# Performance work log

Measured on AMD Instinct MI355X. Metric: run time of the kernel, lower is better.

## Reference

```python
import jax, jax.numpy as jnp
import numpy as np

H, N, F = 10, 200000, 128
HID, C = 256, 100
NEG_SLOPE = 0.2

def _leaky(x):
    return jnp.where(x >= 0, x, NEG_SLOPE * x)

def _prelu(x, a):
    return jnp.where(x >= 0, x, a * x)

def setup_inputs() -> dict:
    key = jax.random.key(0)
    ks = jax.random.split(key, 12)
    inp = {
        "features": jax.random.normal(ks[0], (H, N, F), dtype=jnp.float32),
        "label_emb": jax.random.normal(ks[1], (N, C), dtype=jnp.float32),
        # lr_att: Linear(2F, 1) -> weight as [2F] vector + scalar bias
        "W_att": jax.random.normal(ks[2], (2 * F,), dtype=jnp.float32) * 0.05,
        "b_att": jnp.zeros((), dtype=jnp.float32),
        # lr_output = FeedForwardNetII(F, HID, C, n_layers=2): Dense(F,HID), PReLU, Dense(HID,C)
        "Wo1": jax.random.normal(ks[3], (F, HID), dtype=jnp.float32) * 0.05,
        "bo1": jnp.zeros((HID,), dtype=jnp.float32),
        "ao": jnp.asarray(0.25, dtype=jnp.float32),
        "Wo2": jax.random.normal(ks[4], (HID, C), dtype=jnp.float32) * 0.05,
        "bo2": jnp.zeros((C,), dtype=jnp.float32),
        # label_fc = FeedForwardNet(C, HID, C, n_layers=2): Linear(C,HID), PReLU, Linear(HID,C)
        "Wl1": jax.random.normal(ks[5], (C, HID), dtype=jnp.float32) * 0.05,
        "bl1": jnp.zeros((HID,), dtype=jnp.float32),
        "al": jnp.asarray(0.25, dtype=jnp.float32),
        "Wl2": jax.random.normal(ks[6], (HID, C), dtype=jnp.float32) * 0.05,
        "bl2": jnp.zeros((C,), dtype=jnp.float32),
    }
    return inp

def reference(features, label_emb, W_att, b_att, Wo1, bo1, ao, Wo2, bo2,
              Wl1, bl1, al, Wl2, bl2):
    # features: [H, N, F]; dropouts are identity (p=0, eval mode)
    nF = features.shape[-1]
    W1, W2 = W_att[:nF], W_att[nF:]  # cat([history, x_i]) @ W_att == history@W1 + x_i@W2
    x0 = features[0]
    scores = [_leaky(x0 @ (W1 + W2) + b_att)]  # hop 0: cat([x0, x0])
    for i in range(1, features.shape[0]):
        hist_att = jax.nn.softmax(jnp.stack(scores, axis=1), axis=1)  # [N, i]
        history = jnp.einsum('ni,inf->nf', hist_att, features[:i])    # [N, F]
        scores.append(_leaky(history @ W1 + features[i] @ W2 + b_att))
    att = jax.nn.softmax(jnp.stack(scores, axis=1), axis=1)           # [N, H]
    right = jnp.einsum('ni,inf->nf', att, features)                   # [N, F]
    # lr_output: Dense -> PReLU -> Dense
    out = _prelu(right @ Wo1 + bo1, ao) @ Wo2 + bo2                   # [N, C]
    # label branch: label_fc(label_emb)
    out = out + (_prelu(label_emb @ Wl1 + bl1, al) @ Wl2 + bl2)
    return out
```

## Files before the change

### kernel.cpp

```cpp
#include <hip/hip_runtime.h>
#include <cstddef>

#define NHOP 10
#define NN 200000
#define FF 128
#define HIDD 256
#define CCC 100
#define NEG_SLOPE_C 0.2f

typedef __attribute__((ext_vector_type(8))) short bf16x8;
typedef __attribute__((ext_vector_type(4))) short bf16x4;
typedef __attribute__((ext_vector_type(4))) float f32x4;

__device__ __forceinline__ unsigned short f2bf(float x){
  unsigned u = __float_as_uint(x);
  u = u + 0x7FFFu + ((u >> 16) & 1u);
  return (unsigned short)(u >> 16);
}

__device__ __forceinline__ f32x4 mfma16(bf16x8 a, bf16x8 b, f32x4 c){
  return __builtin_amdgcn_mfma_f32_16x16x32_bf16(a, b, c, 0, 0, 0);
}

__device__ __forceinline__ float leakyf(float x){ return x >= 0.f ? x : NEG_SLOPE_C*x; }

__global__ __launch_bounds__(256) void prep_weights(
    const float* __restrict__ Wo1, const float* __restrict__ Wl1,
    const float* __restrict__ Wo2, const float* __restrict__ Wl2,
    unsigned short* __restrict__ Wo1T, unsigned short* __restrict__ Wl1T,
    unsigned short* __restrict__ Wo2T, unsigned short* __restrict__ Wl2T)
{
  const int id = blockIdx.x*256 + threadIdx.x;
  {
    const int c = id >> 7, k = id & 127;
    Wo1T[id] = f2bf(Wo1[(size_t)k*HIDD + c]);
    Wl1T[id] = (k < CCC) ? f2bf(Wl1[(size_t)k*HIDD + c]) : 0;
  }
  if (id < 112*256){
    const int c = id >> 8, k = id & 255;
    Wo2T[id] = (c < CCC) ? f2bf(Wo2[(size_t)k*CCC + c]) : 0;
    Wl2T[id] = (c < CCC) ? f2bf(Wl2[(size_t)k*CCC + c]) : 0;
  }
}

__global__ __launch_bounds__(256) void attn_right_kernel(
    const float* __restrict__ feat,
    const float* __restrict__ Watt,
    const float* __restrict__ batt,
    unsigned short* __restrict__ rightb)
{
  const int lane = threadIdx.x & 63;
  const int n = blockIdx.x * 4 + (threadIdx.x >> 6);
  if (n >= NN) return;

  const float2 w1 = *reinterpret_cast<const float2*>(Watt + 2*lane);
  const float2 w2 = *reinterpret_cast<const float2*>(Watt + FF + 2*lane);
  const float b = batt[0];

  float2 f[NHOP];
  float p1[NHOP], p2[NHOP];
  const float* fp = feat + (size_t)n*FF + 2*lane;
  #pragma unroll
  for (int i=0;i<NHOP;i++){
    f[i] = *reinterpret_cast<const float2*>(fp + (size_t)i*((size_t)NN*FF));
    p1[i] = f[i].x*w1.x + f[i].y*w1.y;
    p2[i] = f[i].x*w2.x + f[i].y*w2.y;
  }
  #pragma unroll
  for (int m=32;m>0;m>>=1){
    #pragma unroll
    for (int i=0;i<NHOP;i++){
      p1[i] += __shfl_xor(p1[i], m, 64);
      p2[i] += __shfl_xor(p2[i], m, 64);
    }
  }
  float sc[NHOP];
  sc[0] = leakyf(p1[0] + p2[0] + b);
  #pragma unroll
  for (int i=1;i<NHOP;i++){
    float mx = sc[0];
    #pragma unroll
    for (int j=1;j<i;j++) mx = fmaxf(mx, sc[j]);
    float Z = 0.f, hs = 0.f;
    #pragma unroll
    for (int j=0;j<i;j++){
      const float e = __expf(sc[j]-mx);
      Z += e;
      hs = fmaf(e, p1[j], hs);
    }
    sc[i] = leakyf(hs/Z + p2[i] + b);
  }
  float mx = sc[0];
  #pragma unroll
  for (int j=1;j<NHOP;j++) mx = fmaxf(mx, sc[j]);
  float Z = 0.f;
  float e[NHOP];
  #pragma unroll
  for (int j=0;j<NHOP;j++){ e[j] = __expf(sc[j]-mx); Z += e[j]; }
  const float inv = 1.f/Z;
  float rx = 0.f, ry = 0.f;
  #pragma unroll
  for (int j=0;j<NHOP;j++){
    const float a = e[j]*inv;
    rx = fmaf(a, f[j].x, rx);
    ry = fmaf(a, f[j].y, ry);
  }
  ushort2 st; st.x = f2bf(rx); st.y = f2bf(ry);
  *reinterpret_cast<ushort2*>(rightb + (size_t)n*FF + 2*lane) = st;
}

__device__ __forceinline__ void mlp_branch(
    const unsigned short* sA, unsigned short* sH,
    const unsigned short* __restrict__ W1T, const float* __restrict__ b1, const float alpha,
    const unsigned short* __restrict__ W2T,
    f32x4 (&o)[2][4], const int w, const int lr, const int lq)
{
  bf16x8 B[4][4];
  float b1c[4];
  #pragma unroll
  for (int ctl=0; ctl<4; ++ctl){
    const int c = (4*w+ctl)*16 + lr;
    b1c[ctl] = b1[c];
    #pragma unroll
    for (int kk=0; kk<4; ++kk)
      B[ctl][kk] = *reinterpret_cast<const bf16x8*>(W1T + (size_t)c*128 + kk*32 + lq*8);
  }
  #pragma unroll
  for (int nt=0; nt<4; ++nt){
    f32x4 h[4];
    #pragma unroll
    for (int ctl=0; ctl<4; ++ctl) h[ctl] = (f32x4){0.f,0.f,0.f,0.f};
    const int row = nt*16 + lr;
    #pragma unroll
    for (int kk=0; kk<4; ++kk){
      const bf16x8 a = *reinterpret_cast<const bf16x8*>(
          (const char*)sA + row*256 + ((kk*64 + lq*16) ^ ((row&7)<<4)));
      #pragma unroll
      for (int ctl=0; ctl<4; ++ctl)
        h[ctl] = mfma16(a, B[ctl][kk], h[ctl]);
    }
    #pragma unroll
    for (int ctl=0; ctl<4; ++ctl){
      const int c = (4*w+ctl)*16 + lr;
      #pragma unroll
      for (int j=0; j<4; ++j){
        float v = h[ctl][j] + b1c[ctl];
        v = v >= 0.f ? v : alpha*v;
        const int n = nt*16 + lq*4 + j;
        *reinterpret_cast<unsigned short*>(
            (char*)sH + n*512 + ((2*c) ^ ((n&7)<<4))) = f2bf(v);
      }
    }
  }
  __syncthreads();
  #pragma unroll
  for (int i2=0; i2<2; ++i2){
    const int ct2 = 2*w + i2;
    if (ct2 < 7){
      bf16x8 b2[8];
      #pragma unroll
      for (int kk=0; kk<8; ++kk)
        b2[kk] = *reinterpret_cast<const bf16x8*>(W2T + (size_t)(ct2*16+lr)*256 + kk*32 + lq*8);
      #pragma unroll
      for (int nt=0; nt<4; ++nt){
        const int row = nt*16 + lr;
        #pragma unroll
        for (int kk=0; kk<8; ++kk){
          const bf16x8 a2 = *reinterpret_cast<const bf16x8*>(
              (const char*)sH + row*512 + ((kk*64 + lq*16) ^ ((row&7)<<4)));
          o[i2][nt] = mfma16(a2, b2[kk], o[i2][nt]);
        }
      }
    }
  }
}

__global__ __launch_bounds__(256) void mlp_mfma_kernel(
    const unsigned short* __restrict__ rightb, const float* __restrict__ label,
    const unsigned short* __restrict__ Wo1T, const float* __restrict__ bo1, const float* __restrict__ aop,
    const unsigned short* __restrict__ Wo2T, const float* __restrict__ bo2,
    const unsigned short* __restrict__ Wl1T, const float* __restrict__ bl1, const float* __restrict__ alp,
    const unsigned short* __restrict__ Wl2T, const float* __restrict__ bl2,
    float* __restrict__ out)
{
  __shared__ __align__(16) unsigned short sA[64*128];
  __shared__ __align__(16) unsigned short sH[64*256];
  const int t = threadIdx.x;
  const int w = t >> 6, lane = t & 63, lr = lane & 15, lq = lane >> 4;
  const size_t nb = (size_t)blockIdx.x * 64;

  f32x4 o[2][4];
  #pragma unroll
  for (int i2=0; i2<2; ++i2){
    const int ct2 = 2*w + i2;
    const int c2 = ct2*16 + lr;
    const float init = (ct2 < 7 && c2 < CCC) ? (bo2[c2] + bl2[c2]) : 0.f;
    #pragma unroll
    for (int nt=0; nt<4; ++nt) o[i2][nt] = (f32x4){init, init, init, init};
  }

  {
    const unsigned short* src = rightb + nb*FF;
    #pragma unroll
    for (int i=0;i<4;i++){
      const int chunk = t + 256*i;
      const int row = chunk >> 4, cs = chunk & 15;
      const bf16x8 v = *reinterpret_cast<const bf16x8*>(src + row*FF + cs*8);
      *reinterpret_cast<bf16x8*>((char*)sA + row*256 + ((cs*16) ^ ((row&7)<<4))) = v;
    }
  }
  __syncthreads();
  mlp_branch(sA, sH, Wo1T, bo1, aop[0], Wo2T, o, w, lr, lq);

  {
    #pragma unroll
    for (int i=0;i<7;i++){
      const int idx = t + 256*i;
      if (idx < 1600){
        const int row = idx/25, c0 = (idx%25)*4;
        const float4 v = *reinterpret_cast<const float4*>(label + (nb+row)*CCC + c0);
        bf16x4 p;
        p[0] = (short)f2bf(v.x); p[1] = (short)f2bf(v.y);
        p[2] = (short)f2bf(v.z); p[3] = (short)f2bf(v.w);
        *reinterpret_cast<bf16x4*>((char*)sA + row*256 + ((2*c0) ^ ((row&7)<<4))) = p;
      }
    }
    for (int idx = t; idx < 448; idx += 256){
      const int row = idx/7, ch = idx%7;
      *reinterpret_cast<bf16x4*>((char*)sA + row*256 + ((200 + 8*ch) ^ ((row&7)<<4))) = (bf16x4){0,0,0,0};
    }
  }
  __syncthreads();
  mlp_branch(sA, sH, Wl1T, bl1, alp[0], Wl2T, o, w, lr, lq);

  #pragma unroll
  for (int i2=0; i2<2; ++i2){
    const int ct2 = 2*w + i2;
    const int c2 = ct2*16 + lr;
    if (ct2 < 7 && c2 < CCC){
      #pragma unroll
      for (int nt=0; nt<4; ++nt){
        #pragma unroll
        for (int j=0; j<4; ++j){
          const int n = nt*16 + lq*4 + j;
          out[(nb + n)*CCC + c2] = o[i2][nt][j];
        }
      }
    }
  }
}

extern "C" void kernel_launch(void* const* d_in, const int* in_sizes, int n_in,
                              void* d_out, int out_size, void* d_ws, size_t ws_size,
                              hipStream_t stream) {
  const float* feat  = (const float*)d_in[0];
  const float* label = (const float*)d_in[1];
  const float* Watt  = (const float*)d_in[2];
  const float* batt  = (const float*)d_in[3];
  const float* Wo1   = (const float*)d_in[4];
  const float* bo1   = (const float*)d_in[5];
  const float* aop   = (const float*)d_in[6];
  const float* Wo2   = (const float*)d_in[7];
  const float* bo2   = (const float*)d_in[8];
  const float* Wl1   = (const float*)d_in[9];
  const float* bl1   = (const float*)d_in[10];
  const float* alp   = (const float*)d_in[11];
  const float* Wl2   = (const float*)d_in[12];
  const float* bl2   = (const float*)d_in[13];
  float* out = (float*)d_out;

  unsigned short* rightb = (unsigned short*)d_ws;
  unsigned short* Wo1T = rightb + (size_t)NN*FF;
  unsigned short* Wl1T = Wo1T + 256*128;
  unsigned short* Wo2T = Wl1T + 256*128;
  unsigned short* Wl2T = Wo2T + 112*256;

  prep_weights<<<128, 256, 0, stream>>>(Wo1, Wl1, Wo2, Wl2, Wo1T, Wl1T, Wo2T, Wl2T);
  attn_right_kernel<<<NN/4, 256, 0, stream>>>(feat, Watt, batt, rightb);
  mlp_mfma_kernel<<<NN/64, 256, 0, stream>>>(rightb, label,
                                             Wo1T, bo1, aop, Wo2T, bo2,
                                             Wl1T, bl1, alp, Wl2T, bl2, out);
}
```

Baseline: 416.9 us.

## Pack hop features as bf16 in attention kernel and drop MLP staging buffer

```diff
diff --git a/kernel.cpp b/kernel.cpp
--- a/kernel.cpp
+++ b/kernel.cpp
@@ -17,6 +17,9 @@
   u = u + 0x7FFFu + ((u >> 16) & 1u);
   return (unsigned short)(u >> 16);
 }
+__device__ __forceinline__ float bf2f(short s){
+  return __uint_as_float(((unsigned)(unsigned short)s) << 16);
+}
 
 __device__ __forceinline__ f32x4 mfma16(bf16x8 a, bf16x8 b, f32x4 c){
   return __builtin_amdgcn_mfma_f32_16x16x32_bf16(a, b, c, 0, 0, 0);
@@ -50,24 +53,35 @@
     unsigned short* __restrict__ rightb)
 {
   const int lane = threadIdx.x & 63;
-  const int n = blockIdx.x * 4 + (threadIdx.x >> 6);
-  if (n >= NN) return;
-
-  const float2 w1 = *reinterpret_cast<const float2*>(Watt + 2*lane);
-  const float2 w2 = *reinterpret_cast<const float2*>(Watt + FF + 2*lane);
+  const int w = threadIdx.x >> 6;
+  const int nl = lane >> 4, fl = lane & 15;
+  const int n = blockIdx.x*16 + w*4 + nl;
+
+  const float4 w1a = *reinterpret_cast<const float4*>(Watt + fl*4);
+  const float4 w1b = *reinterpret_cast<const float4*>(Watt + 64 + fl*4);
+  const float4 w2a = *reinterpret_cast<const float4*>(Watt + FF + fl*4);
+  const float4 w2b = *reinterpret_cast<const float4*>(Watt + FF + 64 + fl*4);
   const float b = batt[0];
 
-  float2 f[NHOP];
   float p1[NHOP], p2[NHOP];
-  const float* fp = feat + (size_t)n*FF + 2*lane;
+  bf16x8 fbf[NHOP];
+  const float* fp = feat + (size_t)n*FF;
   #pragma unroll
   for (int i=0;i<NHOP;i++){
-    f[i] = *reinterpret_cast<const float2*>(fp + (size_t)i*((size_t)NN*FF));
-    p1[i] = f[i].x*w1.x + f[i].y*w1.y;
-    p2[i] = f[i].x*w2.x + f[i].y*w2.y;
-  }
-  #pragma unroll
-  for (int m=32;m>0;m>>=1){
+    const float* hp = fp + (size_t)i*((size_t)NN*FF);
+    const float4 va = *reinterpret_cast<const float4*>(hp + fl*4);
+    const float4 vb = *reinterpret_cast<const float4*>(hp + 64 + fl*4);
+    p1[i] = va.x*w1a.x + va.y*w1a.y + va.z*w1a.z + va.w*w1a.w
+          + vb.x*w1b.x + vb.y*w1b.y + vb.z*w1b.z + vb.w*w1b.w;
+    p2[i] = va.x*w2a.x + va.y*w2a.y + va.z*w2a.z + va.w*w2a.w
+          + vb.x*w2b.x + vb.y*w2b.y + vb.z*w2b.z + vb.w*w2b.w;
+    fbf[i][0]=(short)f2bf(va.x); fbf[i][1]=(short)f2bf(va.y);
+    fbf[i][2]=(short)f2bf(va.z); fbf[i][3]=(short)f2bf(va.w);
+    fbf[i][4]=(short)f2bf(vb.x); fbf[i][5]=(short)f2bf(vb.y);
+    fbf[i][6]=(short)f2bf(vb.z); fbf[i][7]=(short)f2bf(vb.w);
+  }
+  #pragma unroll
+  for (int m=8;m>0;m>>=1){
     #pragma unroll
     for (int i=0;i<NHOP;i++){
       p1[i] += __shfl_xor(p1[i], m, 64);
@@ -98,61 +112,40 @@
   #pragma unroll
   for (int j=0;j<NHOP;j++){ e[j] = __expf(sc[j]-mx); Z += e[j]; }
   const float inv = 1.f/Z;
-  float rx = 0.f, ry = 0.f;
+  float racc[8];
+  #pragma unroll
+  for (int u=0;u<8;u++) racc[u] = 0.f;
   #pragma unroll
   for (int j=0;j<NHOP;j++){
     const float a = e[j]*inv;
-    rx = fmaf(a, f[j].x, rx);
-    ry = fmaf(a, f[j].y, ry);
-  }
-  ushort2 st; st.x = f2bf(rx); st.y = f2bf(ry);
-  *reinterpret_cast<ushort2*>(rightb + (size_t)n*FF + 2*lane) = st;
-}
-
-__device__ __forceinline__ void mlp_branch(
-    const unsigned short* sA, unsigned short* sH,
-    const unsigned short* __restrict__ W1T, const float* __restrict__ b1, const float alpha,
-    const unsigned short* __restrict__ W2T,
-    f32x4 (&o)[2][4], const int w, const int lr, const int lq)
-{
-  bf16x8 B[4][4];
-  float b1c[4];
-  #pragma unroll
-  for (int ctl=0; ctl<4; ++ctl){
-    const int c = (4*w+ctl)*16 + lr;
-    b1c[ctl] = b1[c];
-    #pragma unroll
-    for (int kk=0; kk<4; ++kk)
-      B[ctl][kk] = *reinterpret_cast<const bf16x8*>(W1T + (size_t)c*128 + kk*32 + lq*8);
-  }
-  #pragma unroll
-  for (int nt=0; nt<4; ++nt){
-    f32x4 h[4];
-    #pragma unroll
-    for (int ctl=0; ctl<4; ++ctl) h[ctl] = (f32x4){0.f,0.f,0.f,0.f};
-    const int row = nt*16 + lr;
-    #pragma unroll
-    for (int kk=0; kk<4; ++kk){
-      const bf16x8 a = *reinterpret_cast<const bf16x8*>(
-          (const char*)sA + row*256 + ((kk*64 + lq*16) ^ ((row&7)<<4)));
-      #pragma unroll
-      for (int ctl=0; ctl<4; ++ctl)
-        h[ctl] = mfma16(a, B[ctl][kk], h[ctl]);
-    }
-    #pragma unroll
-    for (int ctl=0; ctl<4; ++ctl){
-      const int c = (4*w+ctl)*16 + lr;
-      #pragma unroll
-      for (int j=0; j<4; ++j){
-        float v = h[ctl][j] + b1c[ctl];
-        v = v >= 0.f ? v : alpha*v;
-        const int n = nt*16 + lq*4 + j;
-        *reinterpret_cast<unsigned short*>(
-            (char*)sH + n*512 + ((2*c) ^ ((n&7)<<4))) = f2bf(v);
-      }
-    }
-  }
-  __syncthreads();
+    #pragma unroll
+    for (int u=0;u<8;u++) racc[u] = fmaf(a, bf2f(fbf[j][u]), racc[u]);
+  }
+  bf16x4 sa, sb;
+  sa[0]=(short)f2bf(racc[0]); sa[1]=(short)f2bf(racc[1]);
+  sa[2]=(short)f2bf(racc[2]); sa[3]=(short)f2bf(racc[3]);
+  sb[0]=(short)f2bf(racc[4]); sb[1]=(short)f2bf(racc[5]);
+  sb[2]=(short)f2bf(racc[6]); sb[3]=(short)f2bf(racc[7]);
+  *reinterpret_cast<bf16x4*>(rightb + (size_t)n*FF + fl*4) = sa;
+  *reinterpret_cast<bf16x4*>(rightb + (size_t)n*FF + 64 + fl*4) = sb;
+}
+
+__device__ __forceinline__ void scatter_h(unsigned short* sH, f32x4 h, float bias,
+                                          float alpha, int c, int nt, int lq)
+{
+  #pragma unroll
+  for (int j=0;j<4;++j){
+    float v = h[j] + bias;
+    v = v >= 0.f ? v : alpha*v;
+    const int n = nt*16 + lq*4 + j;
+    *reinterpret_cast<unsigned short*>((char*)sH + n*512 + ((2*c) ^ ((n&7)<<4))) = f2bf(v);
+  }
+}
+
+__device__ __forceinline__ void gemm2_accum(const unsigned short* sH,
+    const unsigned short* __restrict__ W2T, f32x4 (&o)[2][4],
+    const int w, const int lr, const int lq)
+{
   #pragma unroll
   for (int i2=0; i2<2; ++i2){
     const int ct2 = 2*w + i2;
@@ -175,6 +168,23 @@
   }
 }
 
+__device__ __forceinline__ bf16x8 label_frag(const float* __restrict__ label,
+                                             size_t gnode, int kk, int lq)
+{
+  bf16x8 r = (bf16x8){0,0,0,0,0,0,0,0};
+  const float* base = label + gnode*CCC;
+  if (kk < 3){
+    const float4 va = *reinterpret_cast<const float4*>(base + kk*32 + lq*8);
+    const float4 vb = *reinterpret_cast<const float4*>(base + kk*32 + lq*8 + 4);
+    r[0]=(short)f2bf(va.x); r[1]=(short)f2bf(va.y); r[2]=(short)f2bf(va.z); r[3]=(short)f2bf(va.w);
+    r[4]=(short)f2bf(vb.x); r[5]=(short)f2bf(vb.y); r[6]=(short)f2bf(vb.z); r[7]=(short)f2bf(vb.w);
+  } else if (lq == 0){
+    const float4 va = *reinterpret_cast<const float4*>(base + 96);
+    r[0]=(short)f2bf(va.x); r[1]=(short)f2bf(va.y); r[2]=(short)f2bf(va.z); r[3]=(short)f2bf(va.w);
+  }
+  return r;
+}
+
 __global__ __launch_bounds__(256) void mlp_mfma_kernel(
     const unsigned short* __restrict__ rightb, const float* __restrict__ label,
     const unsigned short* __restrict__ Wo1T, const float* __restrict__ bo1, const float* __restrict__ aop,
@@ -183,11 +193,11 @@
     const unsigned short* __restrict__ Wl2T, const float* __restrict__ bl2,
     float* __restrict__ out)
 {
-  __shared__ __align__(16) unsigned short sA[64*128];
   __shared__ __align__(16) unsigned short sH[64*256];
   const int t = threadIdx.x;
   const int w = t >> 6, lane = t & 63, lr = lane & 15, lq = lane >> 4;
   const size_t nb = (size_t)blockIdx.x * 64;
+  const float ao = aop[0], al = alp[0];
 
   f32x4 o[2][4];
   #pragma unroll
@@ -199,39 +209,65 @@
     for (int nt=0; nt<4; ++nt) o[i2][nt] = (f32x4){init, init, init, init};
   }
 
-  {
-    const unsigned short* src = rightb + nb*FF;
-    #pragma unroll
-    for (int i=0;i<4;i++){
-      const int chunk = t + 256*i;
-      const int row = chunk >> 4, cs = chunk & 15;
-      const bf16x8 v = *reinterpret_cast<const bf16x8*>(src + row*FF + cs*8);
-      *reinterpret_cast<bf16x8*>((char*)sA + row*256 + ((cs*16) ^ ((row&7)<<4))) = v;
+  #pragma unroll
+  for (int cc=0; cc<2; ++cc){
+    bf16x8 B[2][4];
+    float b1c[2];
+    #pragma unroll
+    for (int ct=0; ct<2; ++ct){
+      const int c = (w*4 + cc*2 + ct)*16 + lr;
+      b1c[ct] = bo1[c];
+      #pragma unroll
+      for (int kk=0; kk<4; ++kk)
+        B[ct][kk] = *reinterpret_cast<const bf16x8*>(Wo1T + (size_t)c*128 + kk*32 + lq*8);
+    }
+    #pragma unroll
+    for (int nt=0; nt<4; ++nt){
+      const int row = nt*16 + lr;
+      f32x4 h0 = (f32x4){0.f,0.f,0.f,0.f}, h1 = h0;
+      #pragma unroll
+      for (int kk=0; kk<4; ++kk){
+        const bf16x8 a = *reinterpret_cast<const bf16x8*>(
+            rightb + (nb + row)*FF + kk*32 + lq*8);
+        h0 = mfma16(a, B[0][kk], h0);
+        h1 = mfma16(a, B[1][kk], h1);
+      }
+      scatter_h(sH, h0, b1c[0], ao, (w*4 + cc*2 + 0)*16 + lr, nt, lq);
+      scatter_h(sH, h1, b1c[1], ao, (w*4 + cc*2 + 1)*16 + lr, nt, lq);
     }
   }
   __syncthreads();
-  mlp_branch(sA, sH, Wo1T, bo1, aop[0], Wo2T, o, w, lr, lq);
-
-  {
-    #pragma unroll
-    for (int i=0;i<7;i++){
-      const int idx = t + 256*i;
-      if (idx < 1600){
-        const int row = idx/25, c0 = (idx%25)*4;
-        const float4 v = *reinterpret_cast<const float4*>(label + (nb+row)*CCC + c0);
-        bf16x4 p;
-        p[0] = (short)f2bf(v.x); p[1] = (short)f2bf(v.y);
-        p[2] = (short)f2bf(v.z); p[3] = (short)f2bf(v.w);
-        *reinterpret_cast<bf16x4*>((char*)sA + row*256 + ((2*c0) ^ ((row&7)<<4))) = p;
+  gemm2_accum(sH, Wo2T, o, w, lr, lq);
+  __syncthreads();
+
+  #pragma unroll
+  for (int cc=0; cc<2; ++cc){
+    bf16x8 B[2][4];
+    float b1c[2];
+    #pragma unroll
+    for (int ct=0; ct<2; ++ct){
+      const int c = (w*4 + cc*2 + ct)*16 + lr;
+      b1c[ct] = bl1[c];
+      #pragma unroll
+      for (int kk=0; kk<4; ++kk)
+        B[ct][kk] = *reinterpret_cast<const bf16x8*>(Wl1T + (size_t)c*128 + kk*32 + lq*8);
+    }
+    #pragma unroll
+    for (int nt=0; nt<4; ++nt){
+      const int row = nt*16 + lr;
+      f32x4 h0 = (f32x4){0.f,0.f,0.f,0.f}, h1 = h0;
+      #pragma unroll
+      for (int kk=0; kk<4; ++kk){
+        const bf16x8 a = label_frag(label, nb + row, kk, lq);
+        h0 = mfma16(a, B[0][kk], h0);
+        h1 = mfma16(a, B[1][kk], h1);
       }
-    }
-    for (int idx = t; idx < 448; idx += 256){
-      const int row = idx/7, ch = idx%7;
-      *reinterpret_cast<bf16x4*>((char*)sA + row*256 + ((200 + 8*ch) ^ ((row&7)<<4))) = (bf16x4){0,0,0,0};
+      scatter_h(sH, h0, b1c[0], al, (w*4 + cc*2 + 0)*16 + lr, nt, lq);
+      scatter_h(sH, h1, b1c[1], al, (w*4 + cc*2 + 1)*16 + lr, nt, lq);
     }
   }
   __syncthreads();
-  mlp_branch(sA, sH, Wl1T, bl1, alp[0], Wl2T, o, w, lr, lq);
+  gemm2_accum(sH, Wl2T, o, w, lr, lq);
 
   #pragma unroll
   for (int i2=0; i2<2; ++i2){
@@ -276,7 +312,7 @@
   unsigned short* Wl2T = Wo2T + 112*256;
 
   prep_weights<<<128, 256, 0, stream>>>(Wo1, Wl1, Wo2, Wl2, Wo1T, Wl1T, Wo2T, Wl2T);
-  attn_right_kernel<<<NN/4, 256, 0, stream>>>(feat, Watt, batt, rightb);
+  attn_right_kernel<<<NN/16, 256, 0, stream>>>(feat, Watt, batt, rightb);
   mlp_mfma_kernel<<<NN/64, 256, 0, stream>>>(rightb, label,
                                              Wo1T, bo1, aop, Wo2T, bo2,
                                              Wl1T, bl1, alp, Wl2T, bl2, out);
```

New measurement: 400.3 us. 4.0% less time.

## Load MLP A-fragments directly from global and stage output through LDS

Applied to the files above, without the earlier changes.

```diff
diff --git a/kernel.cpp b/kernel.cpp
--- a/kernel.cpp
+++ b/kernel.cpp
@@ -1,4 +1,5 @@
 #include <hip/hip_runtime.h>
+#include <hip/hip_bf16.h>
 #include <cstddef>
 
 #define NHOP 10
@@ -12,16 +13,12 @@
 typedef __attribute__((ext_vector_type(4))) short bf16x4;
 typedef __attribute__((ext_vector_type(4))) float f32x4;
 
-__device__ __forceinline__ unsigned short f2bf(float x){
-  unsigned u = __float_as_uint(x);
-  u = u + 0x7FFFu + ((u >> 16) & 1u);
-  return (unsigned short)(u >> 16);
-}
-
+__device__ __forceinline__ short f2bfs(float x){
+  return __builtin_bit_cast(short, __float2bfloat16(x));
+}
 __device__ __forceinline__ f32x4 mfma16(bf16x8 a, bf16x8 b, f32x4 c){
   return __builtin_amdgcn_mfma_f32_16x16x32_bf16(a, b, c, 0, 0, 0);
 }
-
 __device__ __forceinline__ float leakyf(float x){ return x >= 0.f ? x : NEG_SLOPE_C*x; }
 
 __global__ __launch_bounds__(256) void prep_weights(
@@ -33,13 +30,13 @@
   const int id = blockIdx.x*256 + threadIdx.x;
   {
     const int c = id >> 7, k = id & 127;
-    Wo1T[id] = f2bf(Wo1[(size_t)k*HIDD + c]);
-    Wl1T[id] = (k < CCC) ? f2bf(Wl1[(size_t)k*HIDD + c]) : 0;
+    Wo1T[id] = (unsigned short)f2bfs(Wo1[(size_t)k*HIDD + c]);
+    Wl1T[id] = (k < CCC) ? (unsigned short)f2bfs(Wl1[(size_t)k*HIDD + c]) : 0;
   }
   if (id < 112*256){
     const int c = id >> 8, k = id & 255;
-    Wo2T[id] = (c < CCC) ? f2bf(Wo2[(size_t)k*CCC + c]) : 0;
-    Wl2T[id] = (c < CCC) ? f2bf(Wl2[(size_t)k*CCC + c]) : 0;
+    Wo2T[id] = (c < CCC) ? (unsigned short)f2bfs(Wo2[(size_t)k*CCC + c]) : 0;
+    Wl2T[id] = (c < CCC) ? (unsigned short)f2bfs(Wl2[(size_t)k*CCC + c]) : 0;
   }
 }
 
@@ -51,7 +48,6 @@
 {
   const int lane = threadIdx.x & 63;
   const int n = blockIdx.x * 4 + (threadIdx.x >> 6);
-  if (n >= NN) return;
 
   const float2 w1 = *reinterpret_cast<const float2*>(Watt + 2*lane);
   const float2 w2 = *reinterpret_cast<const float2*>(Watt + FF + 2*lane);
@@ -105,54 +101,27 @@
     rx = fmaf(a, f[j].x, rx);
     ry = fmaf(a, f[j].y, ry);
   }
-  ushort2 st; st.x = f2bf(rx); st.y = f2bf(ry);
+  ushort2 st; st.x = (unsigned short)f2bfs(rx); st.y = (unsigned short)f2bfs(ry);
   *reinterpret_cast<ushort2*>(rightb + (size_t)n*FF + 2*lane) = st;
 }
 
-__device__ __forceinline__ void mlp_branch(
-    const unsigned short* sA, unsigned short* sH,
-    const unsigned short* __restrict__ W1T, const float* __restrict__ b1, const float alpha,
-    const unsigned short* __restrict__ W2T,
-    f32x4 (&o)[2][4], const int w, const int lr, const int lq)
-{
-  bf16x8 B[4][4];
-  float b1c[4];
-  #pragma unroll
-  for (int ctl=0; ctl<4; ++ctl){
-    const int c = (4*w+ctl)*16 + lr;
-    b1c[ctl] = b1[c];
-    #pragma unroll
-    for (int kk=0; kk<4; ++kk)
-      B[ctl][kk] = *reinterpret_cast<const bf16x8*>(W1T + (size_t)c*128 + kk*32 + lq*8);
-  }
-  #pragma unroll
-  for (int nt=0; nt<4; ++nt){
-    f32x4 h[4];
-    #pragma unroll
-    for (int ctl=0; ctl<4; ++ctl) h[ctl] = (f32x4){0.f,0.f,0.f,0.f};
-    const int row = nt*16 + lr;
-    #pragma unroll
-    for (int kk=0; kk<4; ++kk){
-      const bf16x8 a = *reinterpret_cast<const bf16x8*>(
-          (const char*)sA + row*256 + ((kk*64 + lq*16) ^ ((row&7)<<4)));
-      #pragma unroll
-      for (int ctl=0; ctl<4; ++ctl)
-        h[ctl] = mfma16(a, B[ctl][kk], h[ctl]);
-    }
-    #pragma unroll
-    for (int ctl=0; ctl<4; ++ctl){
-      const int c = (4*w+ctl)*16 + lr;
-      #pragma unroll
-      for (int j=0; j<4; ++j){
-        float v = h[ctl][j] + b1c[ctl];
-        v = v >= 0.f ? v : alpha*v;
-        const int n = nt*16 + lq*4 + j;
-        *reinterpret_cast<unsigned short*>(
-            (char*)sH + n*512 + ((2*c) ^ ((n&7)<<4))) = f2bf(v);
-      }
-    }
-  }
-  __syncthreads();
+__device__ __forceinline__ void scatter_h(unsigned short* sH, f32x4 h, float bias,
+                                          float alpha, int c, int nt, int lq)
+{
+  #pragma unroll
+  for (int j=0;j<4;++j){
+    float v = h[j] + bias;
+    v = v >= 0.f ? v : alpha*v;
+    const int n = nt*16 + lq*4 + j;
+    *reinterpret_cast<unsigned short*>((char*)sH + n*512 + ((2*c) ^ ((n&7)<<4))) =
+        (unsigned short)f2bfs(v);
+  }
+}
+
+__device__ __forceinline__ void gemm2_accum(const unsigned short* sH,
+    const unsigned short* __restrict__ W2T, f32x4 (&o)[2][4],
+    const int w, const int lr, const int lq)
+{
   #pragma unroll
   for (int i2=0; i2<2; ++i2){
     const int ct2 = 2*w + i2;
@@ -175,6 +144,23 @@
   }
 }
 
+__device__ __forceinline__ bf16x8 label_frag(const float* __restrict__ label,
+                                             size_t gnode, int kk, int lq)
+{
+  bf16x8 r = (bf16x8){0,0,0,0,0,0,0,0};
+  const float* base = label + gnode*CCC;
+  if (kk < 3){
+    const float4 va = *reinterpret_cast<const float4*>(base + kk*32 + lq*8);
+    const float4 vb = *reinterpret_cast<const float4*>(base + kk*32 + lq*8 + 4);
+    r[0]=f2bfs(va.x); r[1]=f2bfs(va.y); r[2]=f2bfs(va.z); r[3]=f2bfs(va.w);
+    r[4]=f2bfs(vb.x); r[5]=f2bfs(vb.y); r[6]=f2bfs(vb.z); r[7]=f2bfs(vb.w);
+  } else if (lq == 0){
+    const float4 va = *reinterpret_cast<const float4*>(base + 96);
+    r[0]=f2bfs(va.x); r[1]=f2bfs(va.y); r[2]=f2bfs(va.z); r[3]=f2bfs(va.w);
+  }
+  return r;
+}
+
 __global__ __launch_bounds__(256) void mlp_mfma_kernel(
     const unsigned short* __restrict__ rightb, const float* __restrict__ label,
     const unsigned short* __restrict__ Wo1T, const float* __restrict__ bo1, const float* __restrict__ aop,
@@ -183,11 +169,11 @@
     const unsigned short* __restrict__ Wl2T, const float* __restrict__ bl2,
     float* __restrict__ out)
 {
-  __shared__ __align__(16) unsigned short sA[64*128];
   __shared__ __align__(16) unsigned short sH[64*256];
   const int t = threadIdx.x;
   const int w = t >> 6, lane = t & 63, lr = lane & 15, lq = lane >> 4;
   const size_t nb = (size_t)blockIdx.x * 64;
+  const float ao = aop[0], al = alp[0];
 
   f32x4 o[2][4];
   #pragma unroll
@@ -200,39 +186,76 @@
   }
 
   {
-    const unsigned short* src = rightb + nb*FF;
-    #pragma unroll
-    for (int i=0;i<4;i++){
-      const int chunk = t + 256*i;
-      const int row = chunk >> 4, cs = chunk & 15;
-      const bf16x8 v = *reinterpret_cast<const bf16x8*>(src + row*FF + cs*8);
-      *reinterpret_cast<bf16x8*>((char*)sA + row*256 + ((cs*16) ^ ((row&7)<<4))) = v;
-    }
-  }
-  __syncthreads();
-  mlp_branch(sA, sH, Wo1T, bo1, aop[0], Wo2T, o, w, lr, lq);
+    bf16x8 B1[4][4];
+    float b1c[4];
+    #pragma unroll
+    for (int q=0; q<4; ++q){
+      const int c = (w*4 + q)*16 + lr;
+      b1c[q] = bo1[c];
+      #pragma unroll
+      for (int kk=0; kk<4; ++kk)
+        B1[q][kk] = *reinterpret_cast<const bf16x8*>(Wo1T + (size_t)c*128 + kk*32 + lq*8);
+    }
+    #pragma unroll
+    for (int nt=0; nt<4; ++nt){
+      const int row = nt*16 + lr;
+      bf16x8 a[4];
+      #pragma unroll
+      for (int kk=0; kk<4; ++kk)
+        a[kk] = *reinterpret_cast<const bf16x8*>(rightb + (nb + row)*FF + kk*32 + lq*8);
+      f32x4 h[4];
+      #pragma unroll
+      for (int q=0; q<4; ++q) h[q] = (f32x4){0.f,0.f,0.f,0.f};
+      #pragma unroll
+      for (int kk=0; kk<4; ++kk)
+        #pragma unroll
+        for (int q=0; q<4; ++q)
+          h[q] = mfma16(a[kk], B1[q][kk], h[q]);
+      #pragma unroll
+      for (int q=0; q<4; ++q)
+        scatter_h(sH, h[q], b1c[q], ao, (w*4 + q)*16 + lr, nt, lq);
+    }
+  }
+  __syncthreads();
+  gemm2_accum(sH, Wo2T, o, w, lr, lq);
+  __syncthreads();
 
   {
-    #pragma unroll
-    for (int i=0;i<7;i++){
-      const int idx = t + 256*i;
-      if (idx < 1600){
-        const int row = idx/25, c0 = (idx%25)*4;
-        const float4 v = *reinterpret_cast<const float4*>(label + (nb+row)*CCC + c0);
-        bf16x4 p;
-        p[0] = (short)f2bf(v.x); p[1] = (short)f2bf(v.y);
-        p[2] = (short)f2bf(v.z); p[3] = (short)f2bf(v.w);
-        *reinterpret_cast<bf16x4*>((char*)sA + row*256 + ((2*c0) ^ ((row&7)<<4))) = p;
-      }
-    }
-    for (int idx = t; idx < 448; idx += 256){
-      const int row = idx/7, ch = idx%7;
-      *reinterpret_cast<bf16x4*>((char*)sA + row*256 + ((200 + 8*ch) ^ ((row&7)<<4))) = (bf16x4){0,0,0,0};
-    }
-  }
-  __syncthreads();
-  mlp_branch(sA, sH, Wl1T, bl1, alp[0], Wl2T, o, w, lr, lq);
-
+    bf16x8 B1[4][4];
+    float b1c[4];
+    #pragma unroll
+    for (int q=0; q<4; ++q){
+      const int c = (w*4 + q)*16 + lr;
+      b1c[q] = bl1[c];
+      #pragma unroll
+      for (int kk=0; kk<4; ++kk)
+        B1[q][kk] = *reinterpret_cast<const bf16x8*>(Wl1T + (size_t)c*128 + kk*32 + lq*8);
+    }
+    #pragma unroll
+    for (int nt=0; nt<4; ++nt){
+      const int row = nt*16 + lr;
+      bf16x8 a[4];
+      #pragma unroll
+      for (int kk=0; kk<4; ++kk)
+        a[kk] = label_frag(label, nb + row, kk, lq);
+      f32x4 h[4];
+      #pragma unroll
+      for (int q=0; q<4; ++q) h[q] = (f32x4){0.f,0.f,0.f,0.f};
+      #pragma unroll
+      for (int kk=0; kk<4; ++kk)
+        #pragma unroll
+        for (int q=0; q<4; ++q)
+          h[q] = mfma16(a[kk], B1[q][kk], h[q]);
+      #pragma unroll
+      for (int q=0; q<4; ++q)
+        scatter_h(sH, h[q], b1c[q], al, (w*4 + q)*16 + lr, nt, lq);
+    }
+  }
+  __syncthreads();
+  gemm2_accum(sH, Wl2T, o, w, lr, lq);
+  __syncthreads();
+
+  float* sF = reinterpret_cast<float*>(sH);
   #pragma unroll
   for (int i2=0; i2<2; ++i2){
     const int ct2 = 2*w + i2;
@@ -241,12 +264,16 @@
       #pragma unroll
       for (int nt=0; nt<4; ++nt){
         #pragma unroll
-        for (int j=0; j<4; ++j){
-          const int n = nt*16 + lq*4 + j;
-          out[(nb + n)*CCC + c2] = o[i2][nt][j];
-        }
+        for (int j=0; j<4; ++j)
+          sF[(nt*16 + lq*4 + j)*CCC + c2] = o[i2][nt][j];
       }
     }
+  }
+  __syncthreads();
+  #pragma unroll
+  for (int p=0; p<25; ++p){
+    const int idx = p*256 + t;
+    out[nb*CCC + idx] = sF[idx];
   }
 }
 
```

After: 473.0 us. +13.5%, slower.

## Map 16 lanes per node with float4 loads and bf16 register caching in attention

Applied to the files above, without the earlier changes.

```diff
diff --git a/kernel.cpp b/kernel.cpp
--- a/kernel.cpp
+++ b/kernel.cpp
@@ -1,4 +1,5 @@
 #include <hip/hip_runtime.h>
+#include <hip/hip_bf16.h>
 #include <cstddef>
 
 #define NHOP 10
@@ -12,16 +13,15 @@
 typedef __attribute__((ext_vector_type(4))) short bf16x4;
 typedef __attribute__((ext_vector_type(4))) float f32x4;
 
-__device__ __forceinline__ unsigned short f2bf(float x){
-  unsigned u = __float_as_uint(x);
-  u = u + 0x7FFFu + ((u >> 16) & 1u);
-  return (unsigned short)(u >> 16);
-}
-
+__device__ __forceinline__ short f2bfs(float x){
+  return __builtin_bit_cast(short, __float2bfloat16(x));
+}
+__device__ __forceinline__ float bf2f(short s){
+  return __uint_as_float(((unsigned)(unsigned short)s) << 16);
+}
 __device__ __forceinline__ f32x4 mfma16(bf16x8 a, bf16x8 b, f32x4 c){
   return __builtin_amdgcn_mfma_f32_16x16x32_bf16(a, b, c, 0, 0, 0);
 }
-
 __device__ __forceinline__ float leakyf(float x){ return x >= 0.f ? x : NEG_SLOPE_C*x; }
 
 __global__ __launch_bounds__(256) void prep_weights(
@@ -33,13 +33,13 @@
   const int id = blockIdx.x*256 + threadIdx.x;
   {
     const int c = id >> 7, k = id & 127;
-    Wo1T[id] = f2bf(Wo1[(size_t)k*HIDD + c]);
-    Wl1T[id] = (k < CCC) ? f2bf(Wl1[(size_t)k*HIDD + c]) : 0;
+    Wo1T[id] = (unsigned short)f2bfs(Wo1[(size_t)k*HIDD + c]);
+    Wl1T[id] = (k < CCC) ? (unsigned short)f2bfs(Wl1[(size_t)k*HIDD + c]) : 0;
   }
   if (id < 112*256){
     const int c = id >> 8, k = id & 255;
-    Wo2T[id] = (c < CCC) ? f2bf(Wo2[(size_t)k*CCC + c]) : 0;
-    Wl2T[id] = (c < CCC) ? f2bf(Wl2[(size_t)k*CCC + c]) : 0;
+    Wo2T[id] = (c < CCC) ? (unsigned short)f2bfs(Wo2[(size_t)k*CCC + c]) : 0;
+    Wl2T[id] = (c < CCC) ? (unsigned short)f2bfs(Wl2[(size_t)k*CCC + c]) : 0;
   }
 }
 
@@ -50,24 +50,33 @@
     unsigned short* __restrict__ rightb)
 {
   const int lane = threadIdx.x & 63;
-  const int n = blockIdx.x * 4 + (threadIdx.x >> 6);
-  if (n >= NN) return;
-
-  const float2 w1 = *reinterpret_cast<const float2*>(Watt + 2*lane);
-  const float2 w2 = *reinterpret_cast<const float2*>(Watt + FF + 2*lane);
+  const int w = threadIdx.x >> 6;
+  const int nl = lane >> 4, fl = lane & 15;
+  const int n = blockIdx.x*16 + w*4 + nl;
+
+  const float4 w1a = *reinterpret_cast<const float4*>(Watt + fl*4);
+  const float4 w1b = *reinterpret_cast<const float4*>(Watt + 64 + fl*4);
+  const float4 w2a = *reinterpret_cast<const float4*>(Watt + FF + fl*4);
+  const float4 w2b = *reinterpret_cast<const float4*>(Watt + FF + 64 + fl*4);
   const float b = batt[0];
 
-  float2 f[NHOP];
   float p1[NHOP], p2[NHOP];
-  const float* fp = feat + (size_t)n*FF + 2*lane;
+  bf16x8 fbf[NHOP];
+  const float* fp = feat + (size_t)n*FF;
   #pragma unroll
   for (int i=0;i<NHOP;i++){
-    f[i] = *reinterpret_cast<const float2*>(fp + (size_t)i*((size_t)NN*FF));
-    p1[i] = f[i].x*w1.x + f[i].y*w1.y;
-    p2[i] = f[i].x*w2.x + f[i].y*w2.y;
-  }
-  #pragma unroll
-  for (int m=32;m>0;m>>=1){
+    const float* hp = fp + (size_t)i*((size_t)NN*FF);
+    const float4 va = *reinterpret_cast<const float4*>(hp + fl*4);
+    const float4 vb = *reinterpret_cast<const float4*>(hp + 64 + fl*4);
+    p1[i] = va.x*w1a.x + va.y*w1a.y + va.z*w1a.z + va.w*w1a.w
+          + vb.x*w1b.x + vb.y*w1b.y + vb.z*w1b.z + vb.w*w1b.w;
+    p2[i] = va.x*w2a.x + va.y*w2a.y + va.z*w2a.z + va.w*w2a.w
+          + vb.x*w2b.x + vb.y*w2b.y + vb.z*w2b.z + vb.w*w2b.w;
+    fbf[i][0]=f2bfs(va.x); fbf[i][1]=f2bfs(va.y); fbf[i][2]=f2bfs(va.z); fbf[i][3]=f2bfs(va.w);
+    fbf[i][4]=f2bfs(vb.x); fbf[i][5]=f2bfs(vb.y); fbf[i][6]=f2bfs(vb.z); fbf[i][7]=f2bfs(vb.w);
+  }
+  #pragma unroll
+  for (int m=8;m>0;m>>=1){
     #pragma unroll
     for (int i=0;i<NHOP;i++){
       p1[i] += __shfl_xor(p1[i], m, 64);
@@ -98,15 +107,20 @@
   #pragma unroll
   for (int j=0;j<NHOP;j++){ e[j] = __expf(sc[j]-mx); Z += e[j]; }
   const float inv = 1.f/Z;
-  float rx = 0.f, ry = 0.f;
+  float racc[8];
+  #pragma unroll
+  for (int u=0;u<8;u++) racc[u] = 0.f;
   #pragma unroll
   for (int j=0;j<NHOP;j++){
     const float a = e[j]*inv;
-    rx = fmaf(a, f[j].x, rx);
-    ry = fmaf(a, f[j].y, ry);
-  }
-  ushort2 st; st.x = f2bf(rx); st.y = f2bf(ry);
-  *reinterpret_cast<ushort2*>(rightb + (size_t)n*FF + 2*lane) = st;
+    #pragma unroll
+    for (int u=0;u<8;u++) racc[u] = fmaf(a, bf2f(fbf[j][u]), racc[u]);
+  }
+  bf16x4 sa, sb;
+  sa[0]=f2bfs(racc[0]); sa[1]=f2bfs(racc[1]); sa[2]=f2bfs(racc[2]); sa[3]=f2bfs(racc[3]);
+  sb[0]=f2bfs(racc[4]); sb[1]=f2bfs(racc[5]); sb[2]=f2bfs(racc[6]); sb[3]=f2bfs(racc[7]);
+  *reinterpret_cast<bf16x4*>(rightb + (size_t)n*FF + fl*4) = sa;
+  *reinterpret_cast<bf16x4*>(rightb + (size_t)n*FF + 64 + fl*4) = sb;
 }
 
 __device__ __forceinline__ void mlp_branch(
@@ -148,7 +162,7 @@
         v = v >= 0.f ? v : alpha*v;
         const int n = nt*16 + lq*4 + j;
         *reinterpret_cast<unsigned short*>(
-            (char*)sH + n*512 + ((2*c) ^ ((n&7)<<4))) = f2bf(v);
+            (char*)sH + n*512 + ((2*c) ^ ((n&7)<<4))) = (unsigned short)f2bfs(v);
       }
     }
   }
@@ -220,8 +234,8 @@
         const int row = idx/25, c0 = (idx%25)*4;
         const float4 v = *reinterpret_cast<const float4*>(label + (nb+row)*CCC + c0);
         bf16x4 p;
-        p[0] = (short)f2bf(v.x); p[1] = (short)f2bf(v.y);
-        p[2] = (short)f2bf(v.z); p[3] = (short)f2bf(v.w);
+        p[0] = f2bfs(v.x); p[1] = f2bfs(v.y);
+        p[2] = f2bfs(v.z); p[3] = f2bfs(v.w);
         *reinterpret_cast<bf16x4*>((char*)sA + row*256 + ((2*c0) ^ ((row&7)<<4))) = p;
       }
     }
@@ -276,7 +290,7 @@
   unsigned short* Wl2T = Wo2T + 112*256;
 
   prep_weights<<<128, 256, 0, stream>>>(Wo1, Wl1, Wo2, Wl2, Wo1T, Wl1T, Wo2T, Wl2T);
-  attn_right_kernel<<<NN/4, 256, 0, stream>>>(feat, Watt, batt, rightb);
+  attn_right_kernel<<<NN/16, 256, 0, stream>>>(feat, Watt, batt, rightb);
   mlp_mfma_kernel<<<NN/64, 256, 0, stream>>>(rightb, label,
                                              Wo1T, bo1, aop, Wo2T, bo2,
                                              Wl1T, bl1, alp, Wl2T, bl2, out);
```

After: 346.6 us. -16.9%, faster.
